# Kernel tuning notes

Hardware: AMD Instinct MI355X
Metric: run time of the kernel (lower is better)

Reference implementation:

```python
import jax, jax.numpy as jnp
import numpy as np

CAPACITY_FACTOR = 1.25


def setup_inputs() -> dict:
    key = jax.random.key(0)
    k1, k2, k3, k4, k5, k6 = jax.random.split(key, 6)
    N, d, E, h = 8192, 1024, 8, 2816
    x = jax.random.normal(k1, (N, d), dtype=jnp.float32)
    topK_indices = jax.random.randint(k2, (N,), 0, E, dtype=jnp.int64)
    topK_scores = jax.random.uniform(k3, (N,), dtype=jnp.float32)
    Wg = jax.random.normal(k4, (E, d, h), dtype=jnp.float32) * 0.02
    Wu = jax.random.normal(k5, (E, d, h), dtype=jnp.float32) * 0.02
    Wd = jax.random.normal(k6, (E, h, d), dtype=jnp.float32) * 0.02
    return {"x": x, "topK_indices": topK_indices, "topK_scores": topK_scores,
            "Wg": Wg, "Wu": Wu, "Wd": Wd}


def reference(x, topK_indices, topK_scores, Wg, Wu, Wd):
    # x: [N, d] tokens; topK_indices: [N] top-1 expert ids; per-expert SwiGLU FFN.
    N, d = x.shape
    E = Wg.shape[0]
    capacity = int(CAPACITY_FACTOR * N / E)  # = 1280

    idx = topK_indices.astype(jnp.int32)
    onehot = jax.nn.one_hot(idx, E, dtype=jnp.int32)            # [N, E]
    # position of each token within its expert's queue (first-come-first-served)
    pos = jnp.sum((jnp.cumsum(onehot, axis=0) - 1) * onehot, axis=1)  # [N]
    kept = pos < capacity                                        # dropped tokens pass through

    # flat dispatch slot: expert*capacity + pos for kept tokens, overflow bucket otherwise
    slots = jnp.where(kept, idx * capacity + pos, E * capacity)  # [N]
    buf = jnp.zeros((E * capacity + 1, d), dtype=x.dtype).at[slots].set(x)
    xe = buf[: E * capacity].reshape(E, capacity, d)             # [E, C, d]

    # per-expert SwiGLU FFN (grouped GEMMs)
    hgate = jnp.einsum('ecd,edh->ech', xe, Wg)
    hup = jnp.einsum('ecd,edh->ech', xe, Wu)
    hact = jax.nn.silu(hgate) * hup
    out = jnp.einsum('ech,ehd->ecd', hact, Wd).reshape(E * capacity, d)
    out = jnp.concatenate([out, jnp.zeros((1, d), out.dtype)], axis=0)

    y_tok = out[slots]                                           # gather back per token
    # multiply_gate_scores=True: scale expert output by routing score; dropped -> identity
    y = jnp.where(kept[:, None], y_tok * topK_scores[:, None], x)
    return y
```

## Files before the change

kernel.cpp:

```cpp
#include <hip/hip_runtime.h>
#include <cstdint>
#include <cstddef>

#define N_TOK 8192
#define DIM   1024
#define NEXP  8
#define HID   2816
#define CAP   1280

typedef __bf16 bf16x8 __attribute__((ext_vector_type(8)));
typedef float  floatx4 __attribute__((ext_vector_type(4)));
typedef unsigned short u16x8 __attribute__((ext_vector_type(8)));

__device__ __forceinline__ unsigned short f2bf(float f) {
  return __builtin_bit_cast(unsigned short, (__bf16)f);
}

__device__ __forceinline__ void async16(void* lds, const void* g) {
  __builtin_amdgcn_global_load_lds(
      (const __attribute__((address_space(1))) void*)g,
      (__attribute__((address_space(3))) void*)lds, 16, 0, 0);
}

__device__ __forceinline__ void fence_barrier() {
  asm volatile("" ::: "memory");
  __builtin_amdgcn_s_barrier();
  asm volatile("" ::: "memory");
}

__global__ void route_kernel(const int* __restrict__ idx, int idx_stride,
                             int* __restrict__ slot,
                             int* __restrict__ slot_token,
                             int* __restrict__ counts) {
  __shared__ int hist[256][NEXP];
  const int t = threadIdx.x;
  int loc[NEXP];
#pragma unroll
  for (int e = 0; e < NEXP; e++) loc[e] = 0;
  const int base = t * 32;
  for (int i = 0; i < 32; i++) {
    int e = idx[(base + i) * idx_stride];
    loc[e]++;
  }
#pragma unroll
  for (int e = 0; e < NEXP; e++) hist[t][e] = loc[e];
  __syncthreads();
  if (t < NEXP) {
    int run = 0;
    for (int i = 0; i < 256; i++) { int v = hist[i][t]; hist[i][t] = run; run += v; }
    counts[t] = run < CAP ? run : CAP;
  }
  __syncthreads();
  int b2[NEXP];
#pragma unroll
  for (int e = 0; e < NEXP; e++) b2[e] = hist[t][e];
  for (int i = 0; i < 32; i++) {
    const int n = base + i;
    const int e = idx[n * idx_stride];
    const int p = b2[e]++;
    if (p < CAP) {
      const int s = e * CAP + p;
      slot[n] = s;
      slot_token[s] = n;
    } else {
      slot[n] = -1;
    }
  }
}

__global__ void dispatch_kernel(const float* __restrict__ x,
                                const int* __restrict__ slot,
                                unsigned short* __restrict__ xe,
                                float* __restrict__ y) {
  const int n = blockIdx.x;
  const int t = threadIdx.x;
  const int s = slot[n];
  const float4 v = ((const float4*)(x + (size_t)n * DIM))[t];
  if (s >= 0) {
    ushort4 b;
    b.x = f2bf(v.x); b.y = f2bf(v.y); b.z = f2bf(v.z); b.w = f2bf(v.w);
    ((ushort4*)(xe + (size_t)s * DIM))[t] = b;
  } else {
    ((float4*)(y + (size_t)n * DIM))[t] = v;
  }
}

__global__ __launch_bounds__(256)
void transpose_cvt(const float* __restrict__ in,
                   unsigned short* __restrict__ out,
                   const int R, const int C) {
  __shared__ float tile[64][65];
  const int e = blockIdx.z;
  const float* ib = in + (size_t)e * R * C;
  unsigned short* ob = out + (size_t)e * R * C;
  const int t = threadIdx.x;
  const int c0 = blockIdx.x * 64, r0 = blockIdx.y * 64;
  const int lr = t >> 4;
  const int lc = (t & 15) * 4;
#pragma unroll
  for (int i = 0; i < 4; i++) {
    const float4 v = *(const float4*)(ib + (size_t)(r0 + lr + i * 16) * C + c0 + lc);
    tile[lr + i * 16][lc + 0] = v.x;
    tile[lr + i * 16][lc + 1] = v.y;
    tile[lr + i * 16][lc + 2] = v.z;
    tile[lr + i * 16][lc + 3] = v.w;
  }
  __syncthreads();
  const int oc = t >> 2;
  const int sub = t & 3;
#pragma unroll
  for (int half = 0; half < 2; half++) {
    const int rch = sub + half * 4;
    u16x8 o;
#pragma unroll
    for (int j = 0; j < 8; j++) o[j] = f2bf(tile[rch * 8 + j][oc]);
    *(u16x8*)(ob + (size_t)(c0 + oc) * R + r0 + rch * 8) = o;
  }
}

template <int MH, int BSTRIDE, class S, class TL>
__device__ __forceinline__ void mm_phase(char* sm, int b, int boff,
                                         int rowA, int rowB, int c0,
                                         floatx4 (&acc)[8][2], S&& stage, TL&& tail) {
  bf16x8 af[4][2], bfr[2][2];
  {
    const char* Ab = sm + b * BSTRIDE + MH * 16384 + rowA;
    const char* Bb = sm + b * BSTRIDE + boff + rowB;
#pragma unroll
    for (int mi = 0; mi < 4; mi++) {
      af[mi][0] = *(const bf16x8*)(Ab + mi * 2048 + c0);
      af[mi][1] = *(const bf16x8*)(Ab + mi * 2048 + (c0 ^ 64));
    }
#pragma unroll
    for (int ni = 0; ni < 2; ni++) {
      bfr[ni][0] = *(const bf16x8*)(Bb + ni * 2048 + c0);
      bfr[ni][1] = *(const bf16x8*)(Bb + ni * 2048 + (c0 ^ 64));
    }
  }
  stage();
  asm volatile("" ::: "memory");
  __builtin_amdgcn_s_barrier();
  asm volatile("s_waitcnt lgkmcnt(0)" ::: "memory");
  __builtin_amdgcn_sched_barrier(0);
  __builtin_amdgcn_s_setprio(1);
#pragma unroll
  for (int mi = 0; mi < 4; mi++)
#pragma unroll
    for (int ni = 0; ni < 2; ni++) {
      acc[MH * 4 + mi][ni] = __builtin_amdgcn_mfma_f32_16x16x32_bf16(
          af[mi][0], bfr[ni][0], acc[MH * 4 + mi][ni], 0, 0, 0);
      acc[MH * 4 + mi][ni] = __builtin_amdgcn_mfma_f32_16x16x32_bf16(
          af[mi][1], bfr[ni][1], acc[MH * 4 + mi][ni], 0, 0, 0);
    }
  __builtin_amdgcn_s_setprio(0);
  tail();
  asm volatile("" ::: "memory");
  __builtin_amdgcn_s_barrier();
  asm volatile("" ::: "memory");
}

__global__ __launch_bounds__(512, 2)
void gateup_gemm8(const unsigned short* __restrict__ A,
                  const unsigned short* __restrict__ Bg,
                  const unsigned short* __restrict__ Bu,
                  const int* __restrict__ counts,
                  unsigned short* __restrict__ hact) {
  extern __shared__ __align__(16) char smem[];
  const int bid = blockIdx.x;
  const int xcd = bid & 7;
  const int slotb = bid >> 3;
  const int m = slotb % 5;
  const int cgl = slotb / 5;
  const int cg = xcd + 8 * cgl;
  const int n = cg % 22;
  const int e = cg / 22;

  const int cnt = counts[e];
  const int m0 = m * 256;
  if (m0 >= cnt) return;
  const int n0 = n * 128;

  const int t = threadIdx.x;
  const int lane = t & 63;
  const int w = t >> 6;
  const int wr = w >> 2;
  const int wc = w & 3;
  const int li = lane & 15;
  const int q = lane >> 4;

  const int sr8 = t >> 3;
  const int cLog = (t & 7) ^ (sr8 & 7);
  const unsigned short* aB  = A  + ((size_t)e * CAP + m0 + sr8) * DIM + cLog * 8;
  const unsigned short* bgB = Bg + ((size_t)e * HID + n0 + sr8) * DIM + cLog * 8;
  const unsigned short* buB = Bu + ((size_t)e * HID + n0 + sr8) * DIM + cLog * 8;

  auto stageU = [&](int bb, int uoff, const unsigned short* s0, const unsigned short* s1) {
    async16(smem + bb * 65536 + uoff + t * 16, s0);
    async16(smem + bb * 65536 + uoff + 8192 + t * 16, s1);
  };

  const int rowA = (wr * 64 + li) * 128;
  const int rowB = (wc * 32 + li) * 128;
  const int c0 = (q ^ (li & 7)) * 16;

  floatx4 accg[8][2] = {};
  floatx4 accu[8][2] = {};

  constexpr int NT = DIM / 64;

  stageU(0, 0,     aB,                     aB + (size_t)64 * DIM);
  stageU(0, 32768, bgB,                    bgB + (size_t)64 * DIM);
  stageU(0, 49152, buB,                    buB + (size_t)64 * DIM);
  stageU(0, 16384, aB + (size_t)128 * DIM, aB + (size_t)192 * DIM);
  stageU(1, 0,     aB + 64,                aB + (size_t)64 * DIM + 64);
  stageU(1, 32768, bgB + 64,               bgB + (size_t)64 * DIM + 64);
  asm volatile("s_waitcnt vmcnt(4)" ::: "memory");
  fence_barrier();

#pragma unroll 2
  for (int T = 0; T < NT; T++) {
    const int b = T & 1;
    const int bn = b ^ 1;
    mm_phase<0, 65536>(smem, b, 32768, rowA, rowB, c0, accg,
        [&] {
          if (T + 1 < NT)
            stageU(bn, 49152, buB + (T + 1) * 64,
                              buB + (size_t)64 * DIM + (T + 1) * 64);
        }, [] {});
    mm_phase<0, 65536>(smem, b, 49152, rowA, rowB, c0, accu,
        [&] {
          if (T + 1 < NT)
            stageU(bn, 16384, aB + (size_t)128 * DIM + (T + 1) * 64,
                              aB + (size_t)192 * DIM + (T + 1) * 64);
        }, [] {});
    mm_phase<1, 65536>(smem, b, 32768, rowA, rowB, c0, accg,
        [&] {
          if (T + 2 < NT)
            stageU(b, 0, aB + (T + 2) * 64,
                         aB + (size_t)64 * DIM + (T + 2) * 64);
        }, [] {});
    mm_phase<1, 65536>(smem, b, 49152, rowA, rowB, c0, accu,
        [&] {
          if (T + 2 < NT)
            stageU(b, 32768, bgB + (T + 2) * 64,
                             bgB + (size_t)64 * DIM + (T + 2) * 64);
        },
        [&] {
          if (T + 2 < NT)
            asm volatile("s_waitcnt vmcnt(4)" ::: "memory");
          else if (T + 1 < NT)
            asm volatile("s_waitcnt vmcnt(0)" ::: "memory");
        });
  }

  unsigned short* ob = hact + (size_t)e * CAP * HID;
#pragma unroll
  for (int mh = 0; mh < 2; mh++)
#pragma unroll
    for (int mi = 0; mi < 4; mi++)
#pragma unroll
      for (int r = 0; r < 4; r++) {
        const int row = m0 + mh * 128 + wr * 64 + mi * 16 + q * 4 + r;
        const size_t rb = (size_t)row * HID;
#pragma unroll
        for (int ni = 0; ni < 2; ni++) {
          const int col = n0 + wc * 32 + ni * 16 + li;
          const float g = accg[mh * 4 + mi][ni][r];
          const float u = accu[mh * 4 + mi][ni][r];
          ob[rb + col] = f2bf(g / (1.0f + __expf(-g)) * u);
        }
      }
}

__global__ __launch_bounds__(512, 2)
void down_gemm8(const unsigned short* __restrict__ A,
                const unsigned short* __restrict__ Bt,
                const int* __restrict__ counts,
                const int* __restrict__ slot_token,
                const float* __restrict__ scores,
                float* __restrict__ y) {
  extern __shared__ __align__(16) char smem[];
  const int bid = blockIdx.x;
  const int xcd = bid & 7;
  const int slotb = bid >> 3;
  const int m = slotb % 5;
  const int cgl = slotb / 5;
  const int cg = xcd + 8 * cgl;
  const int n = cg % 8;
  const int e = cg / 8;

  const int cnt = counts[e];
  const int m0 = m * 256;
  if (m0 >= cnt) return;
  const int n0 = n * 128;

  const int t = threadIdx.x;
  const int lane = t & 63;
  const int w = t >> 6;
  const int wr = w >> 2;
  const int wc = w & 3;
  const int li = lane & 15;
  const int q = lane >> 4;

  const int sr8 = t >> 3;
  const int cLog = (t & 7) ^ (sr8 & 7);
  const unsigned short* aB = A  + ((size_t)e * CAP + m0 + sr8) * HID + cLog * 8;
  const unsigned short* bB = Bt + ((size_t)e * DIM + n0 + sr8) * HID + cLog * 8;

  auto stageU = [&](int bb, int uoff, const unsigned short* s0, const unsigned short* s1) {
    async16(smem + bb * 49152 + uoff + t * 16, s0);
    async16(smem + bb * 49152 + uoff + 8192 + t * 16, s1);
  };

  const int rowA = (wr * 64 + li) * 128;
  const int rowB = (wc * 32 + li) * 128;
  const int c0 = (q ^ (li & 7)) * 16;

  floatx4 acc[8][2] = {};

  constexpr int NT = HID / 64;

  stageU(0, 0,     aB,                     aB + (size_t)64 * HID);
  stageU(0, 32768, bB,                     bB + (size_t)64 * HID);
  stageU(0, 16384, aB + (size_t)128 * HID, aB + (size_t)192 * HID);
  stageU(1, 0,     aB + 64,                aB + (size_t)64 * HID + 64);
  asm volatile("s_waitcnt vmcnt(2)" ::: "memory");
  fence_barrier();

#pragma unroll 2
  for (int T = 0; T < NT; T++) {
    const int b = T & 1;
    const int bn = b ^ 1;
    mm_phase<0, 49152>(smem, b, 32768, rowA, rowB, c0, acc,
        [&] {
          if (T + 1 < NT) {
            stageU(bn, 16384, aB + (size_t)128 * HID + (T + 1) * 64,
                              aB + (size_t)192 * HID + (T + 1) * 64);
            stageU(bn, 32768, bB + (T + 1) * 64,
                              bB + (size_t)64 * HID + (T + 1) * 64);
          }
        }, [] {});
    mm_phase<1, 49152>(smem, b, 32768, rowA, rowB, c0, acc,
        [&] {
          if (T + 2 < NT)
            stageU(b, 0, aB + (T + 2) * 64,
                         aB + (size_t)64 * HID + (T + 2) * 64);
        },
        [&] {
          if (T + 2 < NT)
            asm volatile("s_waitcnt vmcnt(2)" ::: "memory");
          else if (T + 1 < NT)
            asm volatile("s_waitcnt vmcnt(0)" ::: "memory");
        });
  }

#pragma unroll
  for (int mh = 0; mh < 2; mh++)
#pragma unroll
    for (int mi = 0; mi < 4; mi++)
#pragma unroll
      for (int r = 0; r < 4; r++) {
        const int row = m0 + mh * 128 + wr * 64 + mi * 16 + q * 4 + r;
        if (row < cnt) {
          const int tok = slot_token[e * CAP + row];
          const float s = scores[tok];
          float* yr = y + (size_t)tok * DIM;
#pragma unroll
          for (int ni = 0; ni < 2; ni++) {
            const int col = n0 + wc * 32 + ni * 16 + li;
            yr[col] = acc[mh * 4 + mi][ni][r] * s;
          }
        }
      }
}

extern "C" void kernel_launch(void* const* d_in, const int* in_sizes, int n_in,
                              void* d_out, int out_size, void* d_ws, size_t ws_size,
                              hipStream_t stream) {
  const float* x      = (const float*)d_in[0];
  const int*   idx    = (const int*)d_in[1];
  const float* scores = (const float*)d_in[2];
  const float* Wg     = (const float*)d_in[3];
  const float* Wu     = (const float*)d_in[4];
  const float* Wd     = (const float*)d_in[5];
  float* y = (float*)d_out;

  const int idx_stride = (in_sizes[1] == 2 * N_TOK) ? 2 : 1;

  char* ws = (char*)d_ws;
  size_t off = 0;
  auto alloc = [&](size_t b) -> char* {
    char* p = ws + off;
    off += (b + 255) & ~(size_t)255;
    return p;
  };
  int* counts            = (int*)alloc(NEXP * 4);
  int* slot              = (int*)alloc((size_t)N_TOK * 4);
  int* slot_token        = (int*)alloc((size_t)NEXP * CAP * 4);
  unsigned short* xe     = (unsigned short*)alloc((size_t)NEXP * CAP * DIM * 2);
  unsigned short* hact   = (unsigned short*)alloc((size_t)NEXP * CAP * HID * 2);
  unsigned short* wg_t   = (unsigned short*)alloc((size_t)NEXP * DIM * HID * 2);
  unsigned short* wu_t   = (unsigned short*)alloc((size_t)NEXP * DIM * HID * 2);
  unsigned short* wd_t   = (unsigned short*)alloc((size_t)NEXP * DIM * HID * 2);
  (void)ws_size; (void)n_in; (void)out_size;

  static bool s_attr_done = false;
  if (!s_attr_done) {
    hipFuncSetAttribute((const void*)gateup_gemm8,
                        hipFuncAttributeMaxDynamicSharedMemorySize, 131072);
    hipFuncSetAttribute((const void*)down_gemm8,
                        hipFuncAttributeMaxDynamicSharedMemorySize, 98304);
    s_attr_done = true;
  }

  route_kernel<<<1, 256, 0, stream>>>(idx, idx_stride, slot, slot_token, counts);
  dispatch_kernel<<<N_TOK, 256, 0, stream>>>(x, slot, xe, y);

  transpose_cvt<<<dim3(HID / 64, DIM / 64, NEXP), 256, 0, stream>>>(Wg, wg_t, DIM, HID);
  transpose_cvt<<<dim3(HID / 64, DIM / 64, NEXP), 256, 0, stream>>>(Wu, wu_t, DIM, HID);
  transpose_cvt<<<dim3(DIM / 64, HID / 64, NEXP), 256, 0, stream>>>(Wd, wd_t, HID, DIM);

  gateup_gemm8<<<8 * 22 * 5, 512, 131072, stream>>>(xe, wg_t, wu_t, counts, hact);
  down_gemm8<<<8 * 8 * 5, 512, 98304, stream>>>(hact, wd_t, counts, slot_token, scores, y);
}
```

Baseline: 586.4 us.

## Restructure gate/up GEMM into two phases and retile down GEMM to 128x128

The gate/up GEMM now loads the gate and up B fragments once per K-step and reuses each A fragment for both products. Each K-step is two barrier phases instead of four, which cuts LDS re-reads of A and the number of synchronisations. The down GEMM moves from 256x128 tiles with 512 threads to 128x128 tiles with 256 threads and a 4x4 MFMA fragment layout per wave. That doubles the block count to improve load balance over the variable per-expert row counts, at the cost of more reloads of the down-projection weights.

```diff
diff --git a/kernel.cpp b/kernel.cpp
--- a/kernel.cpp
+++ b/kernel.cpp
@@ -26,6 +26,10 @@
   asm volatile("" ::: "memory");
   __builtin_amdgcn_s_barrier();
   asm volatile("" ::: "memory");
+}
+
+__device__ __forceinline__ floatx4 mfma16(bf16x8 a, bf16x8 b, floatx4 c) {
+  return __builtin_amdgcn_mfma_f32_16x16x32_bf16(a, b, c, 0, 0, 0);
 }
 
 __global__ void route_kernel(const int* __restrict__ idx, int idx_stride,
@@ -118,49 +122,8 @@
   }
 }
 
-template <int MH, int BSTRIDE, class S, class TL>
-__device__ __forceinline__ void mm_phase(char* sm, int b, int boff,
-                                         int rowA, int rowB, int c0,
-                                         floatx4 (&acc)[8][2], S&& stage, TL&& tail) {
-  bf16x8 af[4][2], bfr[2][2];
-  {
-    const char* Ab = sm + b * BSTRIDE + MH * 16384 + rowA;
-    const char* Bb = sm + b * BSTRIDE + boff + rowB;
-#pragma unroll
-    for (int mi = 0; mi < 4; mi++) {
-      af[mi][0] = *(const bf16x8*)(Ab + mi * 2048 + c0);
-      af[mi][1] = *(const bf16x8*)(Ab + mi * 2048 + (c0 ^ 64));
-    }
-#pragma unroll
-    for (int ni = 0; ni < 2; ni++) {
-      bfr[ni][0] = *(const bf16x8*)(Bb + ni * 2048 + c0);
-      bfr[ni][1] = *(const bf16x8*)(Bb + ni * 2048 + (c0 ^ 64));
-    }
-  }
-  stage();
-  asm volatile("" ::: "memory");
-  __builtin_amdgcn_s_barrier();
-  asm volatile("s_waitcnt lgkmcnt(0)" ::: "memory");
-  __builtin_amdgcn_sched_barrier(0);
-  __builtin_amdgcn_s_setprio(1);
-#pragma unroll
-  for (int mi = 0; mi < 4; mi++)
-#pragma unroll
-    for (int ni = 0; ni < 2; ni++) {
-      acc[MH * 4 + mi][ni] = __builtin_amdgcn_mfma_f32_16x16x32_bf16(
-          af[mi][0], bfr[ni][0], acc[MH * 4 + mi][ni], 0, 0, 0);
-      acc[MH * 4 + mi][ni] = __builtin_amdgcn_mfma_f32_16x16x32_bf16(
-          af[mi][1], bfr[ni][1], acc[MH * 4 + mi][ni], 0, 0, 0);
-    }
-  __builtin_amdgcn_s_setprio(0);
-  tail();
-  asm volatile("" ::: "memory");
-  __builtin_amdgcn_s_barrier();
-  asm volatile("" ::: "memory");
-}
-
 __global__ __launch_bounds__(512, 2)
-void gateup_gemm8(const unsigned short* __restrict__ A,
+void gateup_gemm2(const unsigned short* __restrict__ A,
                   const unsigned short* __restrict__ Bg,
                   const unsigned short* __restrict__ Bu,
                   const int* __restrict__ counts,
@@ -213,7 +176,6 @@
   stageU(0, 49152, buB,                    buB + (size_t)64 * DIM);
   stageU(0, 16384, aB + (size_t)128 * DIM, aB + (size_t)192 * DIM);
   stageU(1, 0,     aB + 64,                aB + (size_t)64 * DIM + 64);
-  stageU(1, 32768, bgB + 64,               bgB + (size_t)64 * DIM + 64);
   asm volatile("s_waitcnt vmcnt(4)" ::: "memory");
   fence_barrier();
 
@@ -221,36 +183,76 @@
   for (int T = 0; T < NT; T++) {
     const int b = T & 1;
     const int bn = b ^ 1;
-    mm_phase<0, 65536>(smem, b, 32768, rowA, rowB, c0, accg,
-        [&] {
-          if (T + 1 < NT)
-            stageU(bn, 49152, buB + (T + 1) * 64,
-                              buB + (size_t)64 * DIM + (T + 1) * 64);
-        }, [] {});
-    mm_phase<0, 65536>(smem, b, 49152, rowA, rowB, c0, accu,
-        [&] {
-          if (T + 1 < NT)
-            stageU(bn, 16384, aB + (size_t)128 * DIM + (T + 1) * 64,
-                              aB + (size_t)192 * DIM + (T + 1) * 64);
-        }, [] {});
-    mm_phase<1, 65536>(smem, b, 32768, rowA, rowB, c0, accg,
-        [&] {
-          if (T + 2 < NT)
-            stageU(b, 0, aB + (T + 2) * 64,
-                         aB + (size_t)64 * DIM + (T + 2) * 64);
-        }, [] {});
-    mm_phase<1, 65536>(smem, b, 49152, rowA, rowB, c0, accu,
-        [&] {
-          if (T + 2 < NT)
-            stageU(b, 32768, bgB + (T + 2) * 64,
-                             bgB + (size_t)64 * DIM + (T + 2) * 64);
-        },
-        [&] {
-          if (T + 2 < NT)
-            asm volatile("s_waitcnt vmcnt(4)" ::: "memory");
-          else if (T + 1 < NT)
-            asm volatile("s_waitcnt vmcnt(0)" ::: "memory");
-        });
+    char* sb = smem + b * 65536;
+    bf16x8 bgf[2][2], buf2[2][2];
+    {
+      bf16x8 af[4][2];
+#pragma unroll
+      for (int mi = 0; mi < 4; mi++) {
+        af[mi][0] = *(const bf16x8*)(sb + rowA + mi * 2048 + c0);
+        af[mi][1] = *(const bf16x8*)(sb + rowA + mi * 2048 + (c0 ^ 64));
+      }
+#pragma unroll
+      for (int ni = 0; ni < 2; ni++) {
+        bgf[ni][0]  = *(const bf16x8*)(sb + 32768 + rowB + ni * 2048 + c0);
+        bgf[ni][1]  = *(const bf16x8*)(sb + 32768 + rowB + ni * 2048 + (c0 ^ 64));
+        buf2[ni][0] = *(const bf16x8*)(sb + 49152 + rowB + ni * 2048 + c0);
+        buf2[ni][1] = *(const bf16x8*)(sb + 49152 + rowB + ni * 2048 + (c0 ^ 64));
+      }
+      if (T + 1 < NT) {
+        stageU(bn, 32768, bgB + (T + 1) * 64, bgB + (size_t)64 * DIM + (T + 1) * 64);
+        stageU(bn, 49152, buB + (T + 1) * 64, buB + (size_t)64 * DIM + (T + 1) * 64);
+      }
+      asm volatile("" ::: "memory");
+      __builtin_amdgcn_s_barrier();
+      asm volatile("s_waitcnt lgkmcnt(0)" ::: "memory");
+      __builtin_amdgcn_sched_barrier(0);
+      __builtin_amdgcn_s_setprio(1);
+#pragma unroll
+      for (int mi = 0; mi < 4; mi++)
+#pragma unroll
+        for (int ni = 0; ni < 2; ni++) {
+          accg[mi][ni] = mfma16(af[mi][0], bgf[ni][0], accg[mi][ni]);
+          accg[mi][ni] = mfma16(af[mi][1], bgf[ni][1], accg[mi][ni]);
+          accu[mi][ni] = mfma16(af[mi][0], buf2[ni][0], accu[mi][ni]);
+          accu[mi][ni] = mfma16(af[mi][1], buf2[ni][1], accu[mi][ni]);
+        }
+      __builtin_amdgcn_s_setprio(0);
+      if (T + 1 < NT) asm volatile("s_waitcnt vmcnt(6)" ::: "memory");
+      else            asm volatile("s_waitcnt vmcnt(0)" ::: "memory");
+      fence_barrier();
+    }
+    {
+      bf16x8 af[4][2];
+#pragma unroll
+      for (int mi = 0; mi < 4; mi++) {
+        af[mi][0] = *(const bf16x8*)(sb + 16384 + rowA + mi * 2048 + c0);
+        af[mi][1] = *(const bf16x8*)(sb + 16384 + rowA + mi * 2048 + (c0 ^ 64));
+      }
+      if (T + 1 < NT)
+        stageU(bn, 16384, aB + (size_t)128 * DIM + (T + 1) * 64,
+                          aB + (size_t)192 * DIM + (T + 1) * 64);
+      if (T + 2 < NT)
+        stageU(b, 0, aB + (T + 2) * 64, aB + (size_t)64 * DIM + (T + 2) * 64);
+      asm volatile("" ::: "memory");
+      __builtin_amdgcn_s_barrier();
+      asm volatile("s_waitcnt lgkmcnt(0)" ::: "memory");
+      __builtin_amdgcn_sched_barrier(0);
+      __builtin_amdgcn_s_setprio(1);
+#pragma unroll
+      for (int mi = 0; mi < 4; mi++)
+#pragma unroll
+        for (int ni = 0; ni < 2; ni++) {
+          accg[4 + mi][ni] = mfma16(af[mi][0], bgf[ni][0], accg[4 + mi][ni]);
+          accg[4 + mi][ni] = mfma16(af[mi][1], bgf[ni][1], accg[4 + mi][ni]);
+          accu[4 + mi][ni] = mfma16(af[mi][0], buf2[ni][0], accu[4 + mi][ni]);
+          accu[4 + mi][ni] = mfma16(af[mi][1], buf2[ni][1], accu[4 + mi][ni]);
+        }
+      __builtin_amdgcn_s_setprio(0);
+      if (T + 2 < NT)      asm volatile("s_waitcnt vmcnt(4)" ::: "memory");
+      else if (T + 1 < NT) asm volatile("s_waitcnt vmcnt(2)" ::: "memory");
+      fence_barrier();
+    }
   }
 
   unsigned short* ob = hact + (size_t)e * CAP * HID;
@@ -272,8 +274,8 @@
       }
 }
 
-__global__ __launch_bounds__(512, 2)
-void down_gemm8(const unsigned short* __restrict__ A,
+__global__ __launch_bounds__(256, 2)
+void down_gemm2(const unsigned short* __restrict__ A,
                 const unsigned short* __restrict__ Bt,
                 const int* __restrict__ counts,
                 const int* __restrict__ slot_token,
@@ -283,22 +285,22 @@
   const int bid = blockIdx.x;
   const int xcd = bid & 7;
   const int slotb = bid >> 3;
-  const int m = slotb % 5;
-  const int cgl = slotb / 5;
+  const int m = slotb % 10;
+  const int cgl = slotb / 10;
   const int cg = xcd + 8 * cgl;
   const int n = cg % 8;
   const int e = cg / 8;
 
   const int cnt = counts[e];
-  const int m0 = m * 256;
+  const int m0 = m * 128;
   if (m0 >= cnt) return;
   const int n0 = n * 128;
 
   const int t = threadIdx.x;
   const int lane = t & 63;
   const int w = t >> 6;
-  const int wr = w >> 2;
-  const int wc = w & 3;
+  const int wr = w >> 1;
+  const int wc = w & 1;
   const int li = lane & 15;
   const int q = lane >> 4;
 
@@ -307,71 +309,83 @@
   const unsigned short* aB = A  + ((size_t)e * CAP + m0 + sr8) * HID + cLog * 8;
   const unsigned short* bB = Bt + ((size_t)e * DIM + n0 + sr8) * HID + cLog * 8;
 
-  auto stageU = [&](int bb, int uoff, const unsigned short* s0, const unsigned short* s1) {
-    async16(smem + bb * 49152 + uoff + t * 16, s0);
-    async16(smem + bb * 49152 + uoff + 8192 + t * 16, s1);
+  auto stageA = [&](int bb, int koff) {
+#pragma unroll
+    for (int j = 0; j < 4; j++)
+      async16(smem + bb * 32768 + j * 4096 + t * 16, aB + (size_t)j * 32 * HID + koff);
   };
+  auto stageB = [&](int bb, int koff) {
+#pragma unroll
+    for (int j = 0; j < 4; j++)
+      async16(smem + bb * 32768 + 16384 + j * 4096 + t * 16, bB + (size_t)j * 32 * HID + koff);
+  };
 
   const int rowA = (wr * 64 + li) * 128;
-  const int rowB = (wc * 32 + li) * 128;
+  const int rowB = (wc * 64 + li) * 128;
   const int c0 = (q ^ (li & 7)) * 16;
 
-  floatx4 acc[8][2] = {};
+  floatx4 acc[4][4] = {};
 
   constexpr int NT = HID / 64;
 
-  stageU(0, 0,     aB,                     aB + (size_t)64 * HID);
-  stageU(0, 32768, bB,                     bB + (size_t)64 * HID);
-  stageU(0, 16384, aB + (size_t)128 * HID, aB + (size_t)192 * HID);
-  stageU(1, 0,     aB + 64,                aB + (size_t)64 * HID + 64);
-  asm volatile("s_waitcnt vmcnt(2)" ::: "memory");
+  stageA(0, 0);
+  stageB(0, 0);
+  stageA(1, 64);
+  asm volatile("s_waitcnt vmcnt(4)" ::: "memory");
   fence_barrier();
 
 #pragma unroll 2
   for (int T = 0; T < NT; T++) {
     const int b = T & 1;
     const int bn = b ^ 1;
-    mm_phase<0, 49152>(smem, b, 32768, rowA, rowB, c0, acc,
-        [&] {
-          if (T + 1 < NT) {
-            stageU(bn, 16384, aB + (size_t)128 * HID + (T + 1) * 64,
-                              aB + (size_t)192 * HID + (T + 1) * 64);
-            stageU(bn, 32768, bB + (T + 1) * 64,
-                              bB + (size_t)64 * HID + (T + 1) * 64);
-          }
-        }, [] {});
-    mm_phase<1, 49152>(smem, b, 32768, rowA, rowB, c0, acc,
-        [&] {
-          if (T + 2 < NT)
-            stageU(b, 0, aB + (T + 2) * 64,
-                         aB + (size_t)64 * HID + (T + 2) * 64);
-        },
-        [&] {
-          if (T + 2 < NT)
-            asm volatile("s_waitcnt vmcnt(2)" ::: "memory");
-          else if (T + 1 < NT)
-            asm volatile("s_waitcnt vmcnt(0)" ::: "memory");
-        });
-  }
-
-#pragma unroll
-  for (int mh = 0; mh < 2; mh++)
+    char* sb = smem + b * 32768;
+    bf16x8 af[4][2], bfr[4][2];
+#pragma unroll
+    for (int mi = 0; mi < 4; mi++) {
+      af[mi][0] = *(const bf16x8*)(sb + rowA + mi * 2048 + c0);
+      af[mi][1] = *(const bf16x8*)(sb + rowA + mi * 2048 + (c0 ^ 64));
+    }
+#pragma unroll
+    for (int ni = 0; ni < 4; ni++) {
+      bfr[ni][0] = *(const bf16x8*)(sb + 16384 + rowB + ni * 2048 + c0);
+      bfr[ni][1] = *(const bf16x8*)(sb + 16384 + rowB + ni * 2048 + (c0 ^ 64));
+    }
+    if (T + 1 < NT) stageB(bn, (T + 1) * 64);
+    asm volatile("" ::: "memory");
+    __builtin_amdgcn_s_barrier();
+    asm volatile("s_waitcnt lgkmcnt(0)" ::: "memory");
+    __builtin_amdgcn_sched_barrier(0);
+    __builtin_amdgcn_s_setprio(1);
 #pragma unroll
     for (int mi = 0; mi < 4; mi++)
 #pragma unroll
-      for (int r = 0; r < 4; r++) {
-        const int row = m0 + mh * 128 + wr * 64 + mi * 16 + q * 4 + r;
-        if (row < cnt) {
-          const int tok = slot_token[e * CAP + row];
-          const float s = scores[tok];
-          float* yr = y + (size_t)tok * DIM;
-#pragma unroll
-          for (int ni = 0; ni < 2; ni++) {
-            const int col = n0 + wc * 32 + ni * 16 + li;
-            yr[col] = acc[mh * 4 + mi][ni][r] * s;
-          }
+      for (int ni = 0; ni < 4; ni++) {
+        acc[mi][ni] = mfma16(af[mi][0], bfr[ni][0], acc[mi][ni]);
+        acc[mi][ni] = mfma16(af[mi][1], bfr[ni][1], acc[mi][ni]);
+      }
+    __builtin_amdgcn_s_setprio(0);
+    if (T + 2 < NT) stageA(b, (T + 2) * 64);
+    if (T + 2 < NT)      asm volatile("s_waitcnt vmcnt(4)" ::: "memory");
+    else if (T + 1 < NT) asm volatile("s_waitcnt vmcnt(0)" ::: "memory");
+    fence_barrier();
+  }
+
+#pragma unroll
+  for (int mi = 0; mi < 4; mi++)
+#pragma unroll
+    for (int r = 0; r < 4; r++) {
+      const int row = m0 + wr * 64 + mi * 16 + q * 4 + r;
+      if (row < cnt) {
+        const int tok = slot_token[e * CAP + row];
+        const float s = scores[tok];
+        float* yr = y + (size_t)tok * DIM;
+#pragma unroll
+        for (int ni = 0; ni < 4; ni++) {
+          const int col = n0 + wc * 64 + ni * 16 + li;
+          yr[col] = acc[mi][ni][r] * s;
         }
       }
+    }
 }
 
 extern "C" void kernel_launch(void* const* d_in, const int* in_sizes, int n_in,
@@ -406,10 +420,10 @@
 
   static bool s_attr_done = false;
   if (!s_attr_done) {
-    hipFuncSetAttribute((const void*)gateup_gemm8,
+    hipFuncSetAttribute((const void*)gateup_gemm2,
                         hipFuncAttributeMaxDynamicSharedMemorySize, 131072);
-    hipFuncSetAttribute((const void*)down_gemm8,
-                        hipFuncAttributeMaxDynamicSharedMemorySize, 98304);
+    hipFuncSetAttribute((const void*)down_gemm2,
+                        hipFuncAttributeMaxDynamicSharedMemorySize, 65536);
     s_attr_done = true;
   }
 
@@ -420,6 +434,6 @@
   transpose_cvt<<<dim3(HID / 64, DIM / 64, NEXP), 256, 0, stream>>>(Wu, wu_t, DIM, HID);
   transpose_cvt<<<dim3(DIM / 64, HID / 64, NEXP), 256, 0, stream>>>(Wd, wd_t, HID, DIM);
 
-  gateup_gemm8<<<8 * 22 * 5, 512, 131072, stream>>>(xe, wg_t, wu_t, counts, hact);
-  down_gemm8<<<8 * 8 * 5, 512, 98304, stream>>>(hact, wd_t, counts, slot_token, scores, y);
-}
+  gateup_gemm2<<<8 * 22 * 5, 512, 131072, stream>>>(xe, wg_t, wu_t, counts, hact);
+  down_gemm2<<<8 * 8 * 10, 256, 65536, stream>>>(hact, wd_t, counts, slot_token, scores, y);
+}
```

New measurement: 549.0 us. 1.07x faster.
